# Optimization experiments

Measured on AMD Instinct MI355X. Metric: run time of the kernel, lower is better.

Reference implementation:

```python
import jax, jax.numpy as jnp
from jax import lax
import numpy as np

B, NUM_TPM, NUM_CNV, NODE_DIM, DRUG_FEAT = 32, 16000, 16000, 36, 75
N_DRUGS, N_ATOMS, N_PAIRS = 128, 64, 4096


def setup_inputs() -> dict:
    key = jax.random.key(0)
    ks = jax.random.split(key, 32)

    def w(k, shape):
        fan_in = shape[0] if len(shape) == 2 else int(np.prod(shape[1:]))
        return (jax.random.normal(k, shape, jnp.float32) / np.float32(np.sqrt(fan_in))).astype(jnp.float32)

    pic_dim = jax.random.normal(ks[0], (B, 3, 256, 256), jnp.float32)
    rna_seq = jax.random.normal(ks[1], (B, NUM_TPM), jnp.float32)
    gene_cnv = jax.random.normal(ks[2], (B, NUM_CNV), jnp.float32)
    drug_fea = jax.random.uniform(ks[3], (N_DRUGS, N_ATOMS, DRUG_FEAT), jnp.float32)
    a = (jax.random.uniform(ks[4], (N_DRUGS, N_ATOMS, N_ATOMS)) < 0.15).astype(jnp.float32)
    drug_adj = jnp.maximum(a, jnp.transpose(a, (0, 2, 1)))
    index_list = jnp.stack([
        jax.random.randint(ks[5], (N_PAIRS,), 0, B),
        jax.random.randint(ks[6], (N_PAIRS,), 0, N_DRUGS)], axis=1)
    target = jax.random.randint(ks[7], (N_PAIRS,), 0, 2)
    logit_scale = jnp.asarray(10.0, jnp.float32)
    return dict(
        pic_dim=pic_dim, rna_seq=rna_seq, gene_cnv=gene_cnv,
        drug_fea=drug_fea, drug_adj=drug_adj, index_list=index_list,
        target=target, logit_scale=logit_scale,
        conv_w=w(ks[8], (32, 3, 5, 5)), conv_b=jnp.zeros((32,), jnp.float32),
        fc1_w=w(ks[9], (32 * 128 * 128, 1024)), fc1_b=jnp.zeros((1024,), jnp.float32),
        fc2_w=w(ks[10], (1024, 36)), fc2_b=jnp.zeros((36,), jnp.float32),
        mlp1_w1=w(ks[11], (NUM_TPM, NUM_TPM // 4)), mlp1_b1=jnp.zeros((NUM_TPM // 4,), jnp.float32),
        mlp1_w2=w(ks[12], (NUM_TPM // 4, NODE_DIM)), mlp1_b2=jnp.zeros((NODE_DIM,), jnp.float32),
        mlp2_w1=w(ks[13], (NUM_CNV, NUM_CNV // 4)), mlp2_b1=jnp.zeros((NUM_CNV // 4,), jnp.float32),
        mlp2_w2=w(ks[14], (NUM_CNV // 4, NODE_DIM)), mlp2_b2=jnp.zeros((NODE_DIM,), jnp.float32),
        att_w1=w(ks[15], (36, 128)), att_b1=jnp.zeros((128,), jnp.float32),
        att_w2=w(ks[16], (128, 1)),
        end_w1=w(ks[17], (NODE_DIM * 4, NODE_DIM)), end_b1=jnp.zeros((NODE_DIM,), jnp.float32),
        end_w2=w(ks[18], (NODE_DIM, 2)), end_b2=jnp.zeros((2,), jnp.float32),
        gcn_w=w(ks[19], (DRUG_FEAT, NODE_DIM * 8)), gcn_w2=w(ks[20], (NODE_DIM * 8, NODE_DIM * 2)))


def _mlp(x, w1, b1, w2, b2):  # Linear-ReLU-(Dropout eval)-Linear-Softmax
    h = jax.nn.relu(x @ w1 + b1)
    return jax.nn.softmax(h @ w2 + b2, axis=-1)


def _ce(logits, labels):  # mean cross entropy, labels int [N]
    lp = jax.nn.log_softmax(logits, axis=-1)
    return -jnp.take_along_axis(lp, labels[:, None], axis=1).mean()


def reference(pic_dim, rna_seq, gene_cnv, drug_fea, drug_adj, index_list, target,
              logit_scale, conv_w, conv_b, fc1_w, fc1_b, fc2_w, fc2_b,
              mlp1_w1, mlp1_b1, mlp1_w2, mlp1_b2, mlp2_w1, mlp2_b1, mlp2_w2, mlp2_b2,
              att_w1, att_b1, att_w2, end_w1, end_b1, end_w2, end_b2, gcn_w, gcn_w2):
    # omics branches
    rna1 = _mlp(rna_seq, mlp1_w1, mlp1_b1, mlp1_w2, mlp1_b2)    # [B,36]
    cnv1 = _mlp(gene_cnv, mlp2_w1, mlp2_b1, mlp2_w2, mlp2_b2)   # [B,36]
    # image branch: conv(3->32,k5,p2) + relu + maxpool2 + fc
    x = lax.conv_general_dilated(pic_dim, conv_w, (1, 1), [(2, 2), (2, 2)])
    x = jax.nn.relu(x + conv_b[None, :, None, None])
    x = lax.reduce_window(x, -jnp.inf, lax.max, (1, 1, 2, 2), (1, 1, 2, 2), 'VALID')
    x = x.reshape(x.shape[0], -1)                               # [B, 32*128*128]
    x = jax.nn.relu(x @ fc1_w + fc1_b)
    pic1 = x @ fc2_w + fc2_b                                    # [B,36]
    # semantic attention over the two omics views
    z = jnp.stack([rna1, cnv1], axis=1)                         # [B,2,36]
    wv = (jnp.tanh(z @ att_w1 + att_b1) @ att_w2).mean(0)       # [2,1]
    beta = jax.nn.softmax(wv, axis=0)
    cell = (beta[None] * z).sum(1)                              # [B,36]
    # CLIP-style loss
    pic1 = pic1 / jnp.linalg.norm(pic1, axis=1, keepdims=True)
    cell = cell / jnp.linalg.norm(cell, axis=1, keepdims=True)
    image_fea = logit_scale * (pic1 @ cell.T)
    labels = jnp.arange(image_fea.shape[0])
    total_loss2 = (_ce(image_fea, labels) + _ce(image_fea.T, labels)) / 2
    cell_cat = jnp.concatenate([cell, pic1], axis=1)            # [B,72]
    # batched drug GCN (replaces per-drug python loop)
    eye = jnp.eye(N_ATOMS, dtype=jnp.float32)
    def gcn_one(X, A):
        Ht = A.T * (1.0 - eye) + eye        # set diagonal to 1 (add self loops)
        deg = Ht.sum(1)
        dinv = jnp.where(deg == 0, 0.0, 1.0 / deg)
        Hn = dinv[:, None] * Ht             # D^-1 A_hat  (== H.t() after norm)
        out = Hn @ ((Hn @ (X @ gcn_w)) @ gcn_w2)
        return jnp.max(jax.nn.relu(out), axis=0)  # max over atoms -> [72]
    drugfea = jax.vmap(gcn_one)(drug_fea, drug_adj)             # [n_drugs,72]
    # pair prediction head
    Bc = jnp.concatenate([cell_cat[index_list[:, 0]], drugfea[index_list[:, 1]]], axis=1)
    Bp = _mlp(Bc, end_w1, end_b1, end_w2, end_b2)               # [n_pairs,2]
    loss1 = _ce(Bp, target)
    return (loss1, total_loss2, Bp, target)
```

## Files before the change

### kernel.cpp

```cpp
#include <hip/hip_runtime.h>
#include <hip/hip_bf16.h>
#include <math.h>

__device__ __forceinline__ void fma4(float4& a, float s, const float4& v) {
  a.x += s * v.x; a.y += s * v.y; a.z += s * v.z; a.w += s * v.w;
}

__global__ __launch_bounds__(256) void conv_pool_kernel(
    const float* __restrict__ pic, const float* __restrict__ cw,
    const float* __restrict__ cb, float* __restrict__ pooled) {
  __shared__ float tile[3][8][260];
  int bid = blockIdx.x;
  int php = bid & 63, ocg2 = (bid >> 6) & 1, b = bid >> 7;
  int tid = threadIdx.x;
  int pw = tid & 127, phl = tid >> 7;
  int ph = php * 2 + phl;
  int h_base = php * 4 - 2;
  for (int i = tid; i < 3 * 8 * 260; i += 256) {
    int c = i % 260; int rr = (i / 260) & 7; int ic = i / (260 * 8);
    int h = h_base + rr, w = c - 2;
    float v = 0.f;
    if (h >= 0 && h < 256 && w >= 0 && w < 256)
      v = pic[((size_t)b * 3 + ic) * 65536 + h * 256 + w];
    tile[ic][rr][c] = v;
  }
  __syncthreads();
  float acc[16][4];
#pragma unroll
  for (int o = 0; o < 16; ++o)
#pragma unroll
    for (int q = 0; q < 4; ++q) acc[o][q] = 0.f;
  int r0 = phl * 2;
  int c0 = pw * 2;
#pragma unroll
  for (int ic = 0; ic < 3; ++ic) {
    float win[6][6];
#pragma unroll
    for (int r = 0; r < 6; ++r)
#pragma unroll
      for (int cc = 0; cc < 6; ++cc) win[r][cc] = tile[ic][r0 + r][c0 + cc];
#pragma unroll
    for (int o = 0; o < 16; ++o) {
      const float* __restrict__ wk = cw + ((ocg2 * 16 + o) * 3 + ic) * 25;
#pragma unroll
      for (int kh = 0; kh < 5; ++kh)
#pragma unroll
        for (int kw = 0; kw < 5; ++kw) {
          float wv = wk[kh * 5 + kw];
          acc[o][0] += win[kh][kw] * wv;
          acc[o][1] += win[kh][kw + 1] * wv;
          acc[o][2] += win[kh + 1][kw] * wv;
          acc[o][3] += win[kh + 1][kw + 1] * wv;
        }
    }
  }
#pragma unroll
  for (int o = 0; o < 16; ++o) {
    float m = fmaxf(fmaxf(acc[o][0], acc[o][1]), fmaxf(acc[o][2], acc[o][3]));
    m = fmaxf(m + cb[ocg2 * 16 + o], 0.f);
    pooled[(((size_t)b * 32 + ocg2 * 16 + o) * 128 + ph) * 128 + pw] = m;
  }
}

__device__ __forceinline__ void gemm32p_body(
    const float* __restrict__ X, const float* __restrict__ W,
    float* __restrict__ partial, int K, int N, int chunk,
    int bx, int split, float xs[128][36]) {
  int tid = threadIdx.x;
  int colv = bx * 256 + tid;
  int col0 = colv * 4;
  bool active = col0 < N;
  int k0 = split * chunk, k1 = min(k0 + chunk, K);
  size_t Nv = (size_t)(N >> 2);
  const float4* Wv = (const float4*)W;
  float4 acc[32];
#pragma unroll
  for (int b = 0; b < 32; ++b) acc[b] = make_float4(0.f, 0.f, 0.f, 0.f);

  auto fmablk = [&](int kk, const float4& w4) {
    const float4* xr = (const float4*)xs[kk];
#pragma unroll
    for (int b4 = 0; b4 < 8; ++b4) {
      float4 xv = xr[b4];
      fma4(acc[b4 * 4 + 0], xv.x, w4);
      fma4(acc[b4 * 4 + 1], xv.y, w4);
      fma4(acc[b4 * 4 + 2], xv.z, w4);
      fma4(acc[b4 * 4 + 3], xv.w, w4);
    }
  };

  for (int kt = k0; kt < k1; kt += 128) {
    __syncthreads();
    for (int i = tid; i < 4096; i += 256) {
      int b = i >> 7, kk = i & 127;
      xs[kk][b] = X[(size_t)b * K + kt + kk];
    }
    __syncthreads();
    if (active) {
      const float4* wp = Wv + (size_t)kt * Nv + colv;
      float4 cur[8], nxt[8];
#pragma unroll
      for (int j = 0; j < 8; ++j) cur[j] = wp[(size_t)j * Nv];
#pragma unroll 1
      for (int g = 0; g < 15; ++g) {
        const float4* wn = wp + 8 * Nv;
#pragma unroll
        for (int j = 0; j < 8; ++j) nxt[j] = wn[(size_t)j * Nv];
        int kb = g * 8;
#pragma unroll
        for (int j = 0; j < 8; ++j) fmablk(kb + j, cur[j]);
#pragma unroll
        for (int j = 0; j < 8; ++j) cur[j] = nxt[j];
        wp = wn;
      }
#pragma unroll
      for (int j = 0; j < 8; ++j) fmablk(120 + j, cur[j]);
    }
  }
  if (active) {
    float* p = partial + (size_t)split * 32 * N + col0;
#pragma unroll
    for (int b = 0; b < 32; ++b) *(float4*)(p + (size_t)b * N) = acc[b];
  }
}

__global__ __launch_bounds__(256) void gemm32p_kernel(
    const float* __restrict__ X, const float* __restrict__ W,
    float* __restrict__ partial, int K, int N, int chunk) {
  __shared__ float xs[128][36];
  gemm32p_body(X, W, partial, K, N, chunk, blockIdx.x, blockIdx.y, xs);
}

__global__ __launch_bounds__(256) void gemm32p2_kernel(
    const float* __restrict__ X0, const float* __restrict__ W0, float* __restrict__ P0,
    const float* __restrict__ X1, const float* __restrict__ W1, float* __restrict__ P1,
    int K, int N, int chunk) {
  __shared__ float xs[128][36];
  if (blockIdx.z == 0)
    gemm32p_body(X0, W0, P0, K, N, chunk, blockIdx.x, blockIdx.y, xs);
  else
    gemm32p_body(X1, W1, P1, K, N, chunk, blockIdx.x, blockIdx.y, xs);
}

__global__ __launch_bounds__(256) void reduce_s1_kernel(
    const float* __restrict__ partial, float* __restrict__ p2, int N) {
  int i = blockIdx.x * 256 + threadIdx.x;
  if (i >= 32 * N) return;
  int sy = blockIdx.y;
  const float* p = partial + (size_t)(sy * 128) * 32 * N + i;
  size_t st = (size_t)32 * N;
  float s0 = 0, s1 = 0, s2 = 0, s3 = 0, s4 = 0, s5 = 0, s6 = 0, s7 = 0;
  for (int sp = 0; sp < 128; sp += 8) {
    s0 += p[(sp + 0) * st]; s1 += p[(sp + 1) * st];
    s2 += p[(sp + 2) * st]; s3 += p[(sp + 3) * st];
    s4 += p[(sp + 4) * st]; s5 += p[(sp + 5) * st];
    s6 += p[(sp + 6) * st]; s7 += p[(sp + 7) * st];
  }
  p2[(size_t)sy * 32 * N + i] = ((s0 + s1) + (s2 + s3)) + ((s4 + s5) + (s6 + s7));
}

__global__ __launch_bounds__(256) void reduce_s2_kernel(
    const float* __restrict__ p2, const float* __restrict__ bias,
    float* __restrict__ out, int N, int nsy, int relu) {
  int i = blockIdx.x * 256 + threadIdx.x;
  if (i >= 32 * N) return;
  int col = i % N;
  float s = bias[col];
  for (int sy = 0; sy < nsy; ++sy) s += p2[(size_t)sy * 32 * N + i];
  out[i] = relu ? fmaxf(s, 0.f) : s;
}

__device__ __forceinline__ void reduce8_body(
    const float* __restrict__ partial, const float* __restrict__ bias,
    float* __restrict__ out, int N, int nsplit, int relu, int bx) {
  int i = bx * 256 + threadIdx.x;
  if (i >= 32 * N) return;
  int col = i % N;
  const float* p = partial + i;
  size_t st = (size_t)32 * N;
  float s0 = 0, s1 = 0, s2 = 0, s3 = 0, s4 = 0, s5 = 0, s6 = 0, s7 = 0;
  int sp = 0;
  for (; sp + 8 <= nsplit; sp += 8) {
    s0 += p[(sp + 0) * st]; s1 += p[(sp + 1) * st];
    s2 += p[(sp + 2) * st]; s3 += p[(sp + 3) * st];
    s4 += p[(sp + 4) * st]; s5 += p[(sp + 5) * st];
    s6 += p[(sp + 6) * st]; s7 += p[(sp + 7) * st];
  }
  for (; sp < nsplit; ++sp) s0 += p[(size_t)sp * st];
  float s = bias[col] + (((s0 + s1) + (s2 + s3)) + ((s4 + s5) + (s6 + s7)));
  out[i] = relu ? fmaxf(s, 0.f) : s;
}

__global__ __launch_bounds__(256) void reduce2_kernel(
    const float* __restrict__ P0, const float* __restrict__ b0, float* __restrict__ o0,
    const float* __restrict__ P1, const float* __restrict__ b1, float* __restrict__ o1,
    int N, int nsplit, int relu) {
  if (blockIdx.z == 0) reduce8_body(P0, b0, o0, N, nsplit, relu, blockIdx.x);
  else                 reduce8_body(P1, b1, o1, N, nsplit, relu, blockIdx.x);
}

__global__ __launch_bounds__(256) void lin36_all_kernel(
    const float* __restrict__ X0, const float* __restrict__ W0,
    const float* __restrict__ bi0, float* __restrict__ out0,
    const float* __restrict__ X1, const float* __restrict__ W1,
    const float* __restrict__ bi1, float* __restrict__ out1,
    const float* __restrict__ X2, const float* __restrict__ W2,
    const float* __restrict__ bi2, float* __restrict__ out2) {
  const float* X; const float* W; const float* bias; float* out; int K; bool do_sm;
  if (blockIdx.y == 0)      { X = X0; W = W0; bias = bi0; out = out0; K = 4000; do_sm = true; }
  else if (blockIdx.y == 1) { X = X1; W = W1; bias = bi1; out = out1; K = 4000; do_sm = true; }
  else                      { X = X2; W = W2; bias = bi2; out = out2; K = 1024; do_sm = false; }
  __shared__ float xs[4000];
  __shared__ float red[28][36];
  __shared__ float vals[36];
  __shared__ float mxv, smv;
  int b = blockIdx.x, tid = threadIdx.x;
  for (int i = tid; i < K; i += 256) xs[i] = X[(size_t)b * K + i];
  __syncthreads();
  if (tid < 252) {
    int c4 = tid % 9, g = tid / 9;
    const float4* W4 = (const float4*)W;
    float4 s = make_float4(0.f, 0.f, 0.f, 0.f);
    for (int k = g; k < K; k += 28) fma4(s, xs[k], W4[k * 9 + c4]);
    red[g][c4 * 4 + 0] = s.x; red[g][c4 * 4 + 1] = s.y;
    red[g][c4 * 4 + 2] = s.z; red[g][c4 * 4 + 3] = s.w;
  }
  __syncthreads();
  if (tid < 36) {
    float s = bias[tid];
    for (int g = 0; g < 28; ++g) s += red[g][tid];
    vals[tid] = s;
  }
  __syncthreads();
  if (do_sm) {
    if (tid == 0) {
      float m = -1e30f;
      for (int j = 0; j < 36; ++j) m = fmaxf(m, vals[j]);
      float e = 0.f;
      for (int j = 0; j < 36; ++j) e += expf(vals[j] - m);
      mxv = m; smv = e;
    }
    __syncthreads();
    if (tid < 36) out[b * 36 + tid] = expf(vals[tid] - mxv) / smv;
  } else {
    if (tid < 36) out[b * 36 + tid] = vals[tid];
  }
}

__global__ __launch_bounds__(256) void wc_kernel(
    const float* __restrict__ w1, const float* __restrict__ w2, float* __restrict__ wc) {
  int i = blockIdx.x * 256 + threadIdx.x;
  if (i >= 75 * 72) return;
  int r = i / 72, c = i - r * 72;
  float s = 0.f;
  for (int k = 0; k < 288; ++k) s += w1[r * 288 + k] * w2[k * 72 + c];
  wc[i] = s;
}

__global__ __launch_bounds__(256) void gcn_kernel(
    const float* __restrict__ Xg, const float* __restrict__ Ag,
    const float* __restrict__ Wc, float* __restrict__ drugfea) {
  __shared__ float Hn[64][65];
  __shared__ float Xs[64][75];
  __shared__ float Wcs[75][72];
  __shared__ float Ys[64][72];
  __shared__ float Ts[64][72];
  int d = blockIdx.x, tid = threadIdx.x;
  const float* Ad = Ag + (size_t)d * 4096;
  const float* Xd = Xg + (size_t)d * 4800;
  for (int i = tid; i < 4096; i += 256) {
    int r = i & 63, c = i >> 6;
    Hn[r][c] = (r == c) ? 1.f : Ad[c * 64 + r];
  }
  for (int i = tid; i < 4800; i += 256) Xs[i / 75][i % 75] = Xd[i];
  for (int i = tid; i < 5400; i += 256) Wcs[i / 72][i % 72] = Wc[i];
  __syncthreads();
  if (tid < 64) {
    float s = 0.f;
    for (int c = 0; c < 64; ++c) s += Hn[tid][c];
    float inv = (s == 0.f) ? 0.f : 1.f / s;
    for (int c = 0; c < 64; ++c) Hn[tid][c] *= inv;
  }
  __syncthreads();
  int rb = tid >> 3, cb = tid & 7;
  int r0 = rb * 2, c0 = cb * 9;
  {
    float o0[9], o1[9];
#pragma unroll
    for (int j = 0; j < 9; ++j) { o0[j] = 0.f; o1[j] = 0.f; }
    for (int k = 0; k < 75; ++k) {
      float x0 = Xs[r0][k], x1 = Xs[r0 + 1][k];
#pragma unroll
      for (int j = 0; j < 9; ++j) {
        float w = Wcs[k][c0 + j];
        o0[j] += x0 * w; o1[j] += x1 * w;
      }
    }
#pragma unroll
    for (int j = 0; j < 9; ++j) { Ys[r0][c0 + j] = o0[j]; Ys[r0 + 1][c0 + j] = o1[j]; }
  }
  __syncthreads();
  {
    float o0[9], o1[9];
#pragma unroll
    for (int j = 0; j < 9; ++j) { o0[j] = 0.f; o1[j] = 0.f; }
    for (int k = 0; k < 64; ++k) {
      float x0 = Hn[r0][k], x1 = Hn[r0 + 1][k];
#pragma unroll
      for (int j = 0; j < 9; ++j) {
        float w = Ys[k][c0 + j];
        o0[j] += x0 * w; o1[j] += x1 * w;
      }
    }
#pragma unroll
    for (int j = 0; j < 9; ++j) { Ts[r0][c0 + j] = o0[j]; Ts[r0 + 1][c0 + j] = o1[j]; }
  }
  __syncthreads();
  {
    float o0[9], o1[9];
#pragma unroll
    for (int j = 0; j < 9; ++j) { o0[j] = 0.f; o1[j] = 0.f; }
    for (int k = 0; k < 64; ++k) {
      float x0 = Hn[r0][k], x1 = Hn[r0 + 1][k];
#pragma unroll
      for (int j = 0; j < 9; ++j) {
        float w = Ts[k][c0 + j];
        o0[j] += x0 * w; o1[j] += x1 * w;
      }
    }
#pragma unroll
    for (int j = 0; j < 9; ++j) {
      Ys[r0][c0 + j] = fmaxf(o0[j], 0.f);
      Ys[r0 + 1][c0 + j] = fmaxf(o1[j], 0.f);
    }
  }
  __syncthreads();
  if (tid < 72) {
    float m = Ys[0][tid];
    for (int i = 1; i < 64; ++i) m = fmaxf(m, Ys[i][tid]);
    drugfea[d * 72 + tid] = m;
  }
}

__global__ __launch_bounds__(256) void head_kernel(
    const float* __restrict__ rna1, const float* __restrict__ cnv1,
    const float* __restrict__ pic1r, const float* __restrict__ aw1,
    const float* __restrict__ ab1, const float* __restrict__ aw2,
    const float* __restrict__ scale_p, float* __restrict__ cell_cat,
    float* __restrict__ dout) {
  __shared__ float z[2][32][36];
  __shared__ float pic1n[32][36];
  __shared__ float celln[32][36];
  __shared__ float fea[32][32];
  __shared__ float wvp[64];
  __shared__ float beta0, beta1;
  __shared__ float rowl[32], coll[32];
  int tid = threadIdx.x;
  for (int i = tid; i < 1152; i += 256) {
    int b = i / 36, k = i - (i / 36) * 36;
    z[0][b][k] = rna1[i];
    z[1][b][k] = cnv1[i];
    pic1n[b][k] = pic1r[i];
  }
  __syncthreads();
  {
    int p = tid >> 2, sub = tid & 3;
    int b = p >> 1, v = p & 1;
    float s = 0.f;
    for (int h = sub; h < 128; h += 4) {
      float a = ab1[h];
      for (int k = 0; k < 36; ++k) a += z[v][b][k] * aw1[k * 128 + h];
      s += tanhf(a) * aw2[h];
    }
    s += __shfl_down(s, 1, 64);
    s += __shfl_down(s, 2, 64);
    if (sub == 0) wvp[p] = s;
  }
  __syncthreads();
  if (tid == 0) {
    float w0 = 0.f, w1 = 0.f;
    for (int b = 0; b < 32; ++b) { w0 += wvp[b * 2]; w1 += wvp[b * 2 + 1]; }
    w0 /= 32.f; w1 /= 32.f;
    float m = fmaxf(w0, w1);
    float e0 = expf(w0 - m), e1 = expf(w1 - m);
    beta0 = e0 / (e0 + e1); beta1 = e1 / (e0 + e1);
  }
  __syncthreads();
  for (int i = tid; i < 1152; i += 256) {
    int b = i / 36, k = i - (i / 36) * 36;
    celln[b][k] = beta0 * z[0][b][k] + beta1 * z[1][b][k];
  }
  __syncthreads();
  if (tid < 32) {
    float s = 0.f;
    for (int k = 0; k < 36; ++k) { float x = pic1n[tid][k]; s += x * x; }
    float inv = 1.f / sqrtf(s);
    for (int k = 0; k < 36; ++k) pic1n[tid][k] *= inv;
  } else if (tid < 64) {
    int b = tid - 32;
    float s = 0.f;
    for (int k = 0; k < 36; ++k) { float x = celln[b][k]; s += x * x; }
    float inv = 1.f / sqrtf(s);
    for (int k = 0; k < 36; ++k) celln[b][k] *= inv;
  }
  __syncthreads();
  for (int i = tid; i < 1152; i += 256) {
    int b = i / 36, k = i - (i / 36) * 36;
    cell_cat[b * 72 + k] = celln[b][k];
    cell_cat[b * 72 + 36 + k] = pic1n[b][k];
  }
  float sc = *scale_p;
  for (int t = tid; t < 1024; t += 256) {
    int i = t >> 5, j = t & 31;
    float s = 0.f;
    for (int k = 0; k < 36; ++k) s += pic1n[i][k] * celln[j][k];
    fea[i][j] = sc * s;
  }
  __syncthreads();
  if (tid < 32) {
    float m = -1e30f;
    for (int j = 0; j < 32; ++j) m = fmaxf(m, fea[tid][j]);
    float e = 0.f;
    for (int j = 0; j < 32; ++j) e += expf(fea[tid][j] - m);
    rowl[tid] = (logf(e) + m) - fea[tid][tid];
  } else if (tid < 64) {
    int j = tid - 32;
    float m = -1e30f;
    for (int i = 0; i < 32; ++i) m = fmaxf(m, fea[i][j]);
    float e = 0.f;
    for (int i = 0; i < 32; ++i) e += expf(fea[i][j] - m);
    coll[j] = (logf(e) + m) - fea[j][j];
  }
  __syncthreads();
  if (tid == 0) {
    float s1 = 0.f, s2 = 0.f;
    for (int i = 0; i < 32; ++i) { s1 += rowl[i]; s2 += coll[i]; }
    dout[1] = 0.5f * (s1 / 32.f + s2 / 32.f);
  }
}

__global__ __launch_bounds__(256) void pair_kernel(
    const float* __restrict__ cell_cat, const float* __restrict__ drugfea,
    const int* __restrict__ idx, const int* __restrict__ target,
    const float* __restrict__ w1, const float* __restrict__ b1,
    const float* __restrict__ w2, const float* __restrict__ b2,
    float* __restrict__ bp_out, float* __restrict__ tgt_out,
    float* __restrict__ blocksums) {
  __shared__ float w1s[144][36];
  __shared__ float ccs[32][73];
  __shared__ float dfs[128][73];
  __shared__ float w2s[72], b2s[2];
  __shared__ float lsum[256];
  int tid = threadIdx.x;
  {
    float4* dst = (float4*)&w1s[0][0];
    const float4* src = (const float4*)w1;
    for (int i = tid; i < 1296; i += 256) dst[i] = src[i];
  }
  for (int i = tid; i < 2304; i += 256) ccs[i / 72][i % 72] = cell_cat[i];
  for (int i = tid; i < 9216; i += 256) dfs[i / 72][i % 72] = drugfea[i];
  if (tid < 72) w2s[tid] = w2[tid];
  if (tid < 2) b2s[tid] = b2[tid];
  __syncthreads();
  int p = blockIdx.x * 256 + tid;
  int ci = idx[p * 2], dj = idx[p * 2 + 1];
  float4 h4[9];
  {
    const float4* bb = (const float4*)b1;
#pragma unroll
    for (int q = 0; q < 9; ++q) h4[q] = bb[q];
  }
  for (int k = 0; k < 72; ++k) {
    float x = ccs[ci][k];
    const float4* wr = (const float4*)&w1s[k][0];
#pragma unroll
    for (int q = 0; q < 9; ++q) fma4(h4[q], x, wr[q]);
  }
  for (int k = 0; k < 72; ++k) {
    float x = dfs[dj][k];
    const float4* wr = (const float4*)&w1s[72 + k][0];
#pragma unroll
    for (int q = 0; q < 9; ++q) fma4(h4[q], x, wr[q]);
  }
  float l0 = b2s[0], l1 = b2s[1];
#pragma unroll
  for (int q = 0; q < 9; ++q) {
    float hv;
    hv = fmaxf(h4[q].x, 0.f); l0 += hv * w2s[(q * 4 + 0) * 2]; l1 += hv * w2s[(q * 4 + 0) * 2 + 1];
    hv = fmaxf(h4[q].y, 0.f); l0 += hv * w2s[(q * 4 + 1) * 2]; l1 += hv * w2s[(q * 4 + 1) * 2 + 1];
    hv = fmaxf(h4[q].z, 0.f); l0 += hv * w2s[(q * 4 + 2) * 2]; l1 += hv * w2s[(q * 4 + 2) * 2 + 1];
    hv = fmaxf(h4[q].w, 0.f); l0 += hv * w2s[(q * 4 + 3) * 2]; l1 += hv * w2s[(q * 4 + 3) * 2 + 1];
  }
  float m = fmaxf(l0, l1);
  float e0 = expf(l0 - m), e1 = expf(l1 - m);
  float inv = 1.f / (e0 + e1);
  float p0 = e0 * inv, p1 = e1 * inv;
  bp_out[p * 2] = p0;
  bp_out[p * 2 + 1] = p1;
  int t = target[p];
  float mm = fmaxf(p0, p1);
  float lse = logf(expf(p0 - mm) + expf(p1 - mm)) + mm;
  float chosen = t ? p1 : p0;
  lsum[tid] = lse - chosen;
  tgt_out[p] = (float)t;
  __syncthreads();
  for (int s = 128; s > 0; s >>= 1) {
    if (tid < s) lsum[tid] += lsum[tid + s];
    __syncthreads();
  }
  if (tid == 0) blocksums[blockIdx.x] = lsum[0];
}

__global__ void final_kernel(const float* __restrict__ blocksums, float* __restrict__ dout) {
  if (threadIdx.x == 0 && blockIdx.x == 0) {
    float s = 0.f;
    for (int i = 0; i < 16; ++i) s += blocksums[i];
    dout[0] = s / 4096.f;
  }
}

extern "C" void kernel_launch(void* const* d_in, const int* in_sizes, int n_in,
                              void* d_out, int out_size, void* d_ws, size_t ws_size,
                              hipStream_t stream) {
  (void)in_sizes; (void)n_in; (void)out_size; (void)ws_size;
  const float* pic        = (const float*)d_in[0];
  const float* rna        = (const float*)d_in[1];
  const float* cnv        = (const float*)d_in[2];
  const float* drug_fea   = (const float*)d_in[3];
  const float* drug_adj   = (const float*)d_in[4];
  const int*   index_list = (const int*)d_in[5];
  const int*   target     = (const int*)d_in[6];
  const float* logit_scale= (const float*)d_in[7];
  const float* conv_w     = (const float*)d_in[8];
  const float* conv_b     = (const float*)d_in[9];
  const float* fc1_w      = (const float*)d_in[10];
  const float* fc1_b      = (const float*)d_in[11];
  const float* fc2_w      = (const float*)d_in[12];
  const float* fc2_b      = (const float*)d_in[13];
  const float* m1w1       = (const float*)d_in[14];
  const float* m1b1       = (const float*)d_in[15];
  const float* m1w2       = (const float*)d_in[16];
  const float* m1b2       = (const float*)d_in[17];
  const float* m2w1       = (const float*)d_in[18];
  const float* m2b1       = (const float*)d_in[19];
  const float* m2w2       = (const float*)d_in[20];
  const float* m2b2       = (const float*)d_in[21];
  const float* aw1        = (const float*)d_in[22];
  const float* ab1        = (const float*)d_in[23];
  const float* aw2        = (const float*)d_in[24];
  const float* ew1        = (const float*)d_in[25];
  const float* eb1        = (const float*)d_in[26];
  const float* ew2        = (const float*)d_in[27];
  const float* eb2        = (const float*)d_in[28];
  const float* gw         = (const float*)d_in[29];
  const float* gw2        = (const float*)d_in[30];

  float* ws = (float*)d_ws;
  float* pooled  = ws;
  float* pfc1    = ws + 16777216;
  float* p2fc1   = ws + 33554432;
  float* pm1     = ws + 33685504;
  float* pm2     = ws + 41749504;
  float* fcact   = ws + 49813504;
  float* h1      = ws + 49846272;
  float* h2      = ws + 49974272;
  float* rna1    = ws + 50102272;
  float* cnv1    = ws + 50103424;
  float* pic1r   = ws + 50104576;
  float* wcb     = ws + 50105728;
  float* drugf   = ws + 50111128;
  float* cellcat = ws + 50120344;
  float* bsums   = ws + 50122648;

  float* out = (float*)d_out;

  conv_pool_kernel<<<4096, 256, 0, stream>>>(pic, conv_w, conv_b, pooled);
  {
    dim3 g(1, 512);
    gemm32p_kernel<<<g, 256, 0, stream>>>(pooled, fc1_w, pfc1, 524288, 1024, 1024);
    dim3 r1(128, 4);
    reduce_s1_kernel<<<r1, 256, 0, stream>>>(pfc1, p2fc1, 1024);
    reduce_s2_kernel<<<128, 256, 0, stream>>>(p2fc1, fc1_b, fcact, 1024, 4, 1);
  }
  {
    dim3 g(4, 63, 2);
    gemm32p2_kernel<<<g, 256, 0, stream>>>(rna, m1w1, pm1, cnv, m2w1, pm2,
                                           16000, 4000, 256);
    dim3 r(500, 1, 2);
    reduce2_kernel<<<r, 256, 0, stream>>>(pm1, m1b1, h1, pm2, m2b1, h2, 4000, 63, 1);
  }
  {
    dim3 g(32, 3);
    lin36_all_kernel<<<g, 256, 0, stream>>>(h1, m1w2, m1b2, rna1,
                                            h2, m2w2, m2b2, cnv1,
                                            fcact, fc2_w, fc2_b, pic1r);
  }

  wc_kernel<<<22, 256, 0, stream>>>(gw, gw2, wcb);
  gcn_kernel<<<128, 256, 0, stream>>>(drug_fea, drug_adj, wcb, drugf);

  head_kernel<<<1, 256, 0, stream>>>(rna1, cnv1, pic1r, aw1, ab1, aw2,
                                     logit_scale, cellcat, out);

  pair_kernel<<<16, 256, 0, stream>>>(cellcat, drugf, index_list, target,
                                      ew1, eb1, ew2, eb2,
                                      out + 2, out + 2 + 8192, bsums);
  final_kernel<<<1, 64, 0, stream>>>(bsums, out);
}
```

Measured before the change: 1.135 ms.

## Merge independent stages into horizontally fused kernels to cut launches

Combines independent work into shared launches: the conv/pool blocks are interleaved with the two MLP1 split-K GEMMs in one grid, the fc1 stage-1 reduction, the MLP reductions and the Wc precompute share one launch, and the fc1 stage-2 reduction runs alongside the GCN. This removes several kernel launches and the idle tails between dependent-free stages. In exchange, the fused kernels reserve the larger combined shared-memory footprint, which may lower occupancy for the lighter block types.

Result: slower. 1.272 ms (+12.0%).

```diff
diff --git a/kernel.cpp b/kernel.cpp
--- a/kernel.cpp
+++ b/kernel.cpp
@@ -6,11 +6,10 @@
   a.x += s * v.x; a.y += s * v.y; a.z += s * v.z; a.w += s * v.w;
 }
 
-__global__ __launch_bounds__(256) void conv_pool_kernel(
+__device__ __forceinline__ void conv_body(
     const float* __restrict__ pic, const float* __restrict__ cw,
-    const float* __restrict__ cb, float* __restrict__ pooled) {
-  __shared__ float tile[3][8][260];
-  int bid = blockIdx.x;
+    const float* __restrict__ cb, float* __restrict__ pooled,
+    int bid, float tile[3][8][260]) {
   int php = bid & 63, ocg2 = (bid >> 6) & 1, b = bid >> 7;
   int tid = threadIdx.x;
   int pw = tid & 127, phl = tid >> 7;
@@ -124,6 +123,28 @@
   }
 }
 
+__global__ __launch_bounds__(256) void k1_conv_mlp_kernel(
+    const float* __restrict__ pic, const float* __restrict__ cw,
+    const float* __restrict__ cb, float* __restrict__ pooled,
+    const float* __restrict__ rna, const float* __restrict__ m1w1, float* __restrict__ pm1,
+    const float* __restrict__ cnv, const float* __restrict__ m2w1, float* __restrict__ pm2) {
+  __shared__ float xs[128][36];
+  __shared__ float tile[3][8][260];
+  int bid = blockIdx.x;
+  if (bid % 9 == 0) {
+    int j = bid / 9;
+    if (j >= 504) return;
+    int bx = j & 3;
+    int r = j >> 2;
+    int split = r % 63, z = r / 63;
+    if (z == 0) gemm32p_body(rna, m1w1, pm1, 16000, 4000, 256, bx, split, xs);
+    else        gemm32p_body(cnv, m2w1, pm2, 16000, 4000, 256, bx, split, xs);
+  } else {
+    int cbid = bid - bid / 9 - 1;
+    conv_body(pic, cw, cb, pooled, cbid, tile);
+  }
+}
+
 __global__ __launch_bounds__(256) void gemm32p_kernel(
     const float* __restrict__ X, const float* __restrict__ W,
     float* __restrict__ partial, int K, int N, int chunk) {
@@ -131,22 +152,11 @@
   gemm32p_body(X, W, partial, K, N, chunk, blockIdx.x, blockIdx.y, xs);
 }
 
-__global__ __launch_bounds__(256) void gemm32p2_kernel(
-    const float* __restrict__ X0, const float* __restrict__ W0, float* __restrict__ P0,
-    const float* __restrict__ X1, const float* __restrict__ W1, float* __restrict__ P1,
-    int K, int N, int chunk) {
-  __shared__ float xs[128][36];
-  if (blockIdx.z == 0)
-    gemm32p_body(X0, W0, P0, K, N, chunk, blockIdx.x, blockIdx.y, xs);
-  else
-    gemm32p_body(X1, W1, P1, K, N, chunk, blockIdx.x, blockIdx.y, xs);
-}
-
-__global__ __launch_bounds__(256) void reduce_s1_kernel(
-    const float* __restrict__ partial, float* __restrict__ p2, int N) {
-  int i = blockIdx.x * 256 + threadIdx.x;
+__device__ __forceinline__ void reduce_s1_body(
+    const float* __restrict__ partial, float* __restrict__ p2, int N,
+    int bx, int sy) {
+  int i = bx * 256 + threadIdx.x;
   if (i >= 32 * N) return;
-  int sy = blockIdx.y;
   const float* p = partial + (size_t)(sy * 128) * 32 * N + i;
   size_t st = (size_t)32 * N;
   float s0 = 0, s1 = 0, s2 = 0, s3 = 0, s4 = 0, s5 = 0, s6 = 0, s7 = 0;
@@ -157,17 +167,6 @@
     s6 += p[(sp + 6) * st]; s7 += p[(sp + 7) * st];
   }
   p2[(size_t)sy * 32 * N + i] = ((s0 + s1) + (s2 + s3)) + ((s4 + s5) + (s6 + s7));
-}
-
-__global__ __launch_bounds__(256) void reduce_s2_kernel(
-    const float* __restrict__ p2, const float* __restrict__ bias,
-    float* __restrict__ out, int N, int nsy, int relu) {
-  int i = blockIdx.x * 256 + threadIdx.x;
-  if (i >= 32 * N) return;
-  int col = i % N;
-  float s = bias[col];
-  for (int sy = 0; sy < nsy; ++sy) s += p2[(size_t)sy * 32 * N + i];
-  out[i] = relu ? fmaxf(s, 0.f) : s;
 }
 
 __device__ __forceinline__ void reduce8_body(
@@ -191,12 +190,140 @@
   out[i] = relu ? fmaxf(s, 0.f) : s;
 }
 
-__global__ __launch_bounds__(256) void reduce2_kernel(
-    const float* __restrict__ P0, const float* __restrict__ b0, float* __restrict__ o0,
-    const float* __restrict__ P1, const float* __restrict__ b1, float* __restrict__ o1,
-    int N, int nsplit, int relu) {
-  if (blockIdx.z == 0) reduce8_body(P0, b0, o0, N, nsplit, relu, blockIdx.x);
-  else                 reduce8_body(P1, b1, o1, N, nsplit, relu, blockIdx.x);
+__device__ __forceinline__ void wc_body(
+    const float* __restrict__ w1, const float* __restrict__ w2,
+    float* __restrict__ wc, int bx) {
+  int i = bx * 256 + threadIdx.x;
+  if (i >= 75 * 72) return;
+  int r = i / 72, c = i - r * 72;
+  float s = 0.f;
+  for (int k = 0; k < 288; ++k) s += w1[r * 288 + k] * w2[k * 72 + c];
+  wc[i] = s;
+}
+
+__global__ __launch_bounds__(256) void k3_reduce_kernel(
+    const float* __restrict__ pfc1, float* __restrict__ p2fc1,
+    const float* __restrict__ pm1, const float* __restrict__ m1b1, float* __restrict__ h1,
+    const float* __restrict__ pm2, const float* __restrict__ m2b1, float* __restrict__ h2,
+    const float* __restrict__ gw, const float* __restrict__ gw2, float* __restrict__ wcb) {
+  int b = blockIdx.x;
+  if (b < 512) {
+    reduce_s1_body(pfc1, p2fc1, 1024, b & 127, b >> 7);
+  } else if (b < 1512) {
+    int idx = b - 512;
+    if (idx < 500) reduce8_body(pm1, m1b1, h1, 4000, 63, 1, idx);
+    else           reduce8_body(pm2, m2b1, h2, 4000, 63, 1, idx - 500);
+  } else {
+    wc_body(gw, gw2, wcb, b - 1512);
+  }
+}
+
+__device__ __forceinline__ void reduce_s2_body(
+    const float* __restrict__ p2, const float* __restrict__ bias,
+    float* __restrict__ out, int N, int nsy, int relu, int bx) {
+  int i = bx * 256 + threadIdx.x;
+  if (i >= 32 * N) return;
+  int col = i % N;
+  float s = bias[col];
+  for (int sy = 0; sy < nsy; ++sy) s += p2[(size_t)sy * 32 * N + i];
+  out[i] = relu ? fmaxf(s, 0.f) : s;
+}
+
+__device__ __forceinline__ void gcn_body(
+    const float* __restrict__ Xg, const float* __restrict__ Ag,
+    const float* __restrict__ Wc, float* __restrict__ drugfea, int d,
+    float Hn[64][65], float Xs[64][75], float Wcs[75][72],
+    float Ys[64][72], float Ts[64][72]) {
+  int tid = threadIdx.x;
+  const float* Ad = Ag + (size_t)d * 4096;
+  const float* Xd = Xg + (size_t)d * 4800;
+  for (int i = tid; i < 4096; i += 256) {
+    int r = i & 63, c = i >> 6;
+    Hn[r][c] = (r == c) ? 1.f : Ad[c * 64 + r];
+  }
+  for (int i = tid; i < 4800; i += 256) Xs[i / 75][i % 75] = Xd[i];
+  for (int i = tid; i < 5400; i += 256) Wcs[i / 72][i % 72] = Wc[i];
+  __syncthreads();
+  if (tid < 64) {
+    float s = 0.f;
+    for (int c = 0; c < 64; ++c) s += Hn[tid][c];
+    float inv = (s == 0.f) ? 0.f : 1.f / s;
+    for (int c = 0; c < 64; ++c) Hn[tid][c] *= inv;
+  }
+  __syncthreads();
+  int rb = tid >> 3, cb = tid & 7;
+  int r0 = rb * 2, c0 = cb * 9;
+  {
+    float o0[9], o1[9];
+#pragma unroll
+    for (int j = 0; j < 9; ++j) { o0[j] = 0.f; o1[j] = 0.f; }
+    for (int k = 0; k < 75; ++k) {
+      float x0 = Xs[r0][k], x1 = Xs[r0 + 1][k];
+#pragma unroll
+      for (int j = 0; j < 9; ++j) {
+        float w = Wcs[k][c0 + j];
+        o0[j] += x0 * w; o1[j] += x1 * w;
+      }
+    }
+#pragma unroll
+    for (int j = 0; j < 9; ++j) { Ys[r0][c0 + j] = o0[j]; Ys[r0 + 1][c0 + j] = o1[j]; }
+  }
+  __syncthreads();
+  {
+    float o0[9], o1[9];
+#pragma unroll
+    for (int j = 0; j < 9; ++j) { o0[j] = 0.f; o1[j] = 0.f; }
+    for (int k = 0; k < 64; ++k) {
+      float x0 = Hn[r0][k], x1 = Hn[r0 + 1][k];
+#pragma unroll
+      for (int j = 0; j < 9; ++j) {
+        float w = Ys[k][c0 + j];
+        o0[j] += x0 * w; o1[j] += x1 * w;
+      }
+    }
+#pragma unroll
+    for (int j = 0; j < 9; ++j) { Ts[r0][c0 + j] = o0[j]; Ts[r0 + 1][c0 + j] = o1[j]; }
+  }
+  __syncthreads();
+  {
+    float o0[9], o1[9];
+#pragma unroll
+    for (int j = 0; j < 9; ++j) { o0[j] = 0.f; o1[j] = 0.f; }
+    for (int k = 0; k < 64; ++k) {
+      float x0 = Hn[r0][k], x1 = Hn[r0 + 1][k];
+#pragma unroll
+      for (int j = 0; j < 9; ++j) {
+        float w = Ts[k][c0 + j];
+        o0[j] += x0 * w; o1[j] += x1 * w;
+      }
+    }
+#pragma unroll
+    for (int j = 0; j < 9; ++j) {
+      Ys[r0][c0 + j] = fmaxf(o0[j], 0.f);
+      Ys[r0 + 1][c0 + j] = fmaxf(o1[j], 0.f);
+    }
+  }
+  __syncthreads();
+  if (tid < 72) {
+    float m = Ys[0][tid];
+    for (int i = 1; i < 64; ++i) m = fmaxf(m, Ys[i][tid]);
+    drugfea[d * 72 + tid] = m;
+  }
+}
+
+__global__ __launch_bounds__(256) void k4_s2_gcn_kernel(
+    const float* __restrict__ p2fc1, const float* __restrict__ fc1_b,
+    float* __restrict__ fcact,
+    const float* __restrict__ Xg, const float* __restrict__ Ag,
+    const float* __restrict__ wcb, float* __restrict__ drugfea) {
+  __shared__ float Hn[64][65];
+  __shared__ float Xs[64][75];
+  __shared__ float Wcs[75][72];
+  __shared__ float Ys[64][72];
+  __shared__ float Ts[64][72];
+  int b = blockIdx.x;
+  if (b < 128) reduce_s2_body(p2fc1, fc1_b, fcact, 1024, 4, 1, b);
+  else         gcn_body(Xg, Ag, wcb, drugfea, b - 128, Hn, Xs, Wcs, Ys, Ts);
 }
 
 __global__ __launch_bounds__(256) void lin36_all_kernel(
@@ -244,101 +371,6 @@
     if (tid < 36) out[b * 36 + tid] = expf(vals[tid] - mxv) / smv;
   } else {
     if (tid < 36) out[b * 36 + tid] = vals[tid];
-  }
-}
-
-__global__ __launch_bounds__(256) void wc_kernel(
-    const float* __restrict__ w1, const float* __restrict__ w2, float* __restrict__ wc) {
-  int i = blockIdx.x * 256 + threadIdx.x;
-  if (i >= 75 * 72) return;
-  int r = i / 72, c = i - r * 72;
-  float s = 0.f;
-  for (int k = 0; k < 288; ++k) s += w1[r * 288 + k] * w2[k * 72 + c];
-  wc[i] = s;
-}
-
-__global__ __launch_bounds__(256) void gcn_kernel(
-    const float* __restrict__ Xg, const float* __restrict__ Ag,
-    const float* __restrict__ Wc, float* __restrict__ drugfea) {
-  __shared__ float Hn[64][65];
-  __shared__ float Xs[64][75];
-  __shared__ float Wcs[75][72];
-  __shared__ float Ys[64][72];
-  __shared__ float Ts[64][72];
-  int d = blockIdx.x, tid = threadIdx.x;
-  const float* Ad = Ag + (size_t)d * 4096;
-  const float* Xd = Xg + (size_t)d * 4800;
-  for (int i = tid; i < 4096; i += 256) {
-    int r = i & 63, c = i >> 6;
-    Hn[r][c] = (r == c) ? 1.f : Ad[c * 64 + r];
-  }
-  for (int i = tid; i < 4800; i += 256) Xs[i / 75][i % 75] = Xd[i];
-  for (int i = tid; i < 5400; i += 256) Wcs[i / 72][i % 72] = Wc[i];
-  __syncthreads();
-  if (tid < 64) {
-    float s = 0.f;
-    for (int c = 0; c < 64; ++c) s += Hn[tid][c];
-    float inv = (s == 0.f) ? 0.f : 1.f / s;
-    for (int c = 0; c < 64; ++c) Hn[tid][c] *= inv;
-  }
-  __syncthreads();
-  int rb = tid >> 3, cb = tid & 7;
-  int r0 = rb * 2, c0 = cb * 9;
-  {
-    float o0[9], o1[9];
-#pragma unroll
-    for (int j = 0; j < 9; ++j) { o0[j] = 0.f; o1[j] = 0.f; }
-    for (int k = 0; k < 75; ++k) {
-      float x0 = Xs[r0][k], x1 = Xs[r0 + 1][k];
-#pragma unroll
-      for (int j = 0; j < 9; ++j) {
-        float w = Wcs[k][c0 + j];
-        o0[j] += x0 * w; o1[j] += x1 * w;
-      }
-    }
-#pragma unroll
-    for (int j = 0; j < 9; ++j) { Ys[r0][c0 + j] = o0[j]; Ys[r0 + 1][c0 + j] = o1[j]; }
-  }
-  __syncthreads();
-  {
-    float o0[9], o1[9];
-#pragma unroll
-    for (int j = 0; j < 9; ++j) { o0[j] = 0.f; o1[j] = 0.f; }
-    for (int k = 0; k < 64; ++k) {
-      float x0 = Hn[r0][k], x1 = Hn[r0 + 1][k];
-#pragma unroll
-      for (int j = 0; j < 9; ++j) {
-        float w = Ys[k][c0 + j];
-        o0[j] += x0 * w; o1[j] += x1 * w;
-      }
-    }
-#pragma unroll
-    for (int j = 0; j < 9; ++j) { Ts[r0][c0 + j] = o0[j]; Ts[r0 + 1][c0 + j] = o1[j]; }
-  }
-  __syncthreads();
-  {
-    float o0[9], o1[9];
-#pragma unroll
-    for (int j = 0; j < 9; ++j) { o0[j] = 0.f; o1[j] = 0.f; }
-    for (int k = 0; k < 64; ++k) {
-      float x0 = Hn[r0][k], x1 = Hn[r0 + 1][k];
-#pragma unroll
-      for (int j = 0; j < 9; ++j) {
-        float w = Ts[k][c0 + j];
-        o0[j] += x0 * w; o1[j] += x1 * w;
-      }
-    }
-#pragma unroll
-    for (int j = 0; j < 9; ++j) {
-      Ys[r0][c0 + j] = fmaxf(o0[j], 0.f);
-      Ys[r0 + 1][c0 + j] = fmaxf(o1[j], 0.f);
-    }
-  }
-  __syncthreads();
-  if (tid < 72) {
-    float m = Ys[0][tid];
-    for (int i = 1; i < 64; ++i) m = fmaxf(m, Ys[i][tid]);
-    drugfea[d * 72 + tid] = m;
   }
 }
 
@@ -574,34 +606,25 @@
 
   float* out = (float*)d_out;
 
-  conv_pool_kernel<<<4096, 256, 0, stream>>>(pic, conv_w, conv_b, pooled);
+  k1_conv_mlp_kernel<<<4608, 256, 0, stream>>>(pic, conv_w, conv_b, pooled,
+                                               rna, m1w1, pm1, cnv, m2w1, pm2);
   {
     dim3 g(1, 512);
     gemm32p_kernel<<<g, 256, 0, stream>>>(pooled, fc1_w, pfc1, 524288, 1024, 1024);
-    dim3 r1(128, 4);
-    reduce_s1_kernel<<<r1, 256, 0, stream>>>(pfc1, p2fc1, 1024);
-    reduce_s2_kernel<<<128, 256, 0, stream>>>(p2fc1, fc1_b, fcact, 1024, 4, 1);
-  }
-  {
-    dim3 g(4, 63, 2);
-    gemm32p2_kernel<<<g, 256, 0, stream>>>(rna, m1w1, pm1, cnv, m2w1, pm2,
-                                           16000, 4000, 256);
-    dim3 r(500, 1, 2);
-    reduce2_kernel<<<r, 256, 0, stream>>>(pm1, m1b1, h1, pm2, m2b1, h2, 4000, 63, 1);
-  }
+  }
+  k3_reduce_kernel<<<1534, 256, 0, stream>>>(pfc1, p2fc1,
+                                             pm1, m1b1, h1, pm2, m2b1, h2,
+                                             gw, gw2, wcb);
+  k4_s2_gcn_kernel<<<256, 256, 0, stream>>>(p2fc1, fc1_b, fcact,
+                                            drug_fea, drug_adj, wcb, drugf);
   {
     dim3 g(32, 3);
     lin36_all_kernel<<<g, 256, 0, stream>>>(h1, m1w2, m1b2, rna1,
                                             h2, m2w2, m2b2, cnv1,
                                             fcact, fc2_w, fc2_b, pic1r);
   }
-
-  wc_kernel<<<22, 256, 0, stream>>>(gw, gw2, wcb);
-  gcn_kernel<<<128, 256, 0, stream>>>(drug_fea, drug_adj, wcb, drugf);
-
   head_kernel<<<1, 256, 0, stream>>>(rna1, cnv1, pic1r, aw1, ab1, aw2,
                                      logit_scale, cellcat, out);
-
   pair_kernel<<<16, 256, 0, stream>>>(cellcat, drugf, index_list, target,
                                       ew1, eb1, ew2, eb2,
                                       out + 2, out + 2 + 8192, bsums);
```
